# Optimization experiments

Measured on AMD Instinct MI355X. Metric: run time of the kernel, lower is better.

Reference implementation:

```python
import jax, jax.numpy as jnp
import numpy as np

N = 50000
D_IN, D_H1, D_H2 = 256, 128, 64
E = 1_600_000


def setup_inputs() -> dict:
    key = jax.random.key(0)
    k = jax.random.split(key, 6)
    x = jax.random.normal(k[0], (N, D_IN), dtype=jnp.float32)
    edge_index = jax.random.randint(k[1], (2, E), 0, N, dtype=jnp.int64)
    # Glorot-style init like torch_geometric GCNConv (weight [in, out], zero bias)
    W1 = jax.random.normal(k[2], (D_IN, D_H1), dtype=jnp.float32) * (2.0 / (D_IN + D_H1)) ** 0.5
    b1 = jnp.zeros((D_H1,), dtype=jnp.float32)
    W2 = jax.random.normal(k[3], (D_H1, D_H2), dtype=jnp.float32) * (2.0 / (D_H1 + D_H2)) ** 0.5
    b2 = jnp.zeros((D_H2,), dtype=jnp.float32)
    return {"x": x, "edge_index": edge_index, "W1": W1, "b1": b1, "W2": W2, "b2": b2}


def _gcn_norm(edge_index, n):
    # add self-loops, symmetric normalization: D^{-1/2} (A+I) D^{-1/2}
    loops = jnp.arange(n, dtype=edge_index.dtype)
    src = jnp.concatenate([edge_index[0], loops])
    dst = jnp.concatenate([edge_index[1], loops])
    deg = jnp.zeros((n,), jnp.float32).at[dst].add(1.0)
    dinv = jnp.where(deg > 0, jax.lax.rsqrt(deg), 0.0)
    w = dinv[src] * dinv[dst]  # [E+N]
    return src, dst, w


def _gcn_conv(x, W, b, src, dst, w, n):
    z = x @ W  # dense transform first (out_dim < in_dim)
    msg = z[src] * w[:, None]  # gather + scale, [E+N, out]
    out = jax.ops.segment_sum(msg, dst, num_segments=n)  # scatter-add
    return out + b


def reference(x, edge_index, W1, b1, W2, b2):
    src, dst, w = _gcn_norm(edge_index, N)
    z = jax.nn.relu(_gcn_conv(x, W1, b1, src, dst, w, N))
    z = jax.nn.relu(_gcn_conv(z, W2, b2, src, dst, w, N))
    return z
```

## Files before the change

kernel.cpp:

```cpp
#include <hip/hip_runtime.h>
#include <hip/hip_bf16.h>
#include <cstdint>
#include <cstddef>

#define NNODES 50000
#define NEDGES 1600000
#define DIN 256
#define DH1 128
#define DH2 64

#define NBKT 196
#define NCHUNK 128
#define CHUNKE 12500
#define STAGE_CAP 10240

__device__ __forceinline__ float bflo(uint32_t u) { return __uint_as_float(u << 16); }
__device__ __forceinline__ float bfhi(uint32_t u) { return __uint_as_float(u & 0xffff0000u); }
__device__ __forceinline__ uint16_t f2bf(float f) {
    uint32_t u = __float_as_uint(f);
    u += 0x7fffu + ((u >> 16) & 1u);
    return (uint16_t)(u >> 16);
}

using b8 = __attribute__((ext_vector_type(8))) short;
using f4x = __attribute__((ext_vector_type(4))) float;

__global__ __launch_bounds__(256) void k_chunkhist(const int* __restrict__ dst,
                                                   int* __restrict__ counts) {
    __shared__ int hist[NBKT];
    int c = blockIdx.x, t = threadIdx.x;
    if (t < NBKT) hist[t] = 0;
    __syncthreads();
    int e0 = c * CHUNKE, e1 = min(NEDGES, e0 + CHUNKE);
    for (int e = e0 + t; e < e1; e += 256) atomicAdd(&hist[dst[e] >> 8], 1);
    __syncthreads();
    if (t < NBKT) counts[c * NBKT + t] = hist[t];
}

__global__ __launch_bounds__(256) void k_bktscan(int* __restrict__ counts,
                                                 int* __restrict__ bktstart,
                                                 int* __restrict__ bktcnt) {
    __shared__ int lds[256];
    int t = threadIdx.x;
    int total = 0;
    if (t < NBKT)
        for (int c = 0; c < NCHUNK; ++c) total += counts[c * NBKT + t];
    lds[t] = total;
    __syncthreads();
    for (int d = 1; d < 256; d <<= 1) {
        int add = (t >= d) ? lds[t - d] : 0;
        __syncthreads();
        lds[t] += add;
        __syncthreads();
    }
    int base = lds[t] - total;
    if (t < NBKT) {
        bktstart[t] = base;
        bktcnt[t] = total;
        int run = base;
        for (int c = 0; c < NCHUNK; ++c) {
            int x = counts[c * NBKT + t];
            counts[c * NBKT + t] = run;
            run += x;
        }
    }
}

__global__ __launch_bounds__(256) void k_pairscatter(const int* __restrict__ src,
                                                     const int* __restrict__ dst,
                                                     const int* __restrict__ counts,
                                                     uint32_t* __restrict__ pairs) {
    __shared__ int cur[NBKT];
    int c = blockIdx.x, t = threadIdx.x;
    if (t < NBKT) cur[t] = counts[c * NBKT + t];
    __syncthreads();
    int e0 = c * CHUNKE, e1 = min(NEDGES, e0 + CHUNKE);
    for (int e = e0 + t; e < e1; e += 256) {
        int d = dst[e];
        int pos = atomicAdd(&cur[d >> 8], 1);
        pairs[pos] = ((uint32_t)(d & 255) << 16) | (uint32_t)src[e];
    }
}

__global__ __launch_bounds__(256) void k_sortbucket(const uint32_t* __restrict__ pairs,
                                                    const int* __restrict__ bktstart,
                                                    const int* __restrict__ bktcnt,
                                                    int* __restrict__ csr,
                                                    int* __restrict__ off,
                                                    float* __restrict__ dinv) {
    __shared__ int hist[256];
    __shared__ int cur[256];
    __shared__ int stage[STAGE_CAP];
    int b = blockIdx.x, t = threadIdx.x;
    int e0 = bktstart[b], ecnt = bktcnt[b];
    hist[t] = 0;
    __syncthreads();
    for (int e = e0 + t; e < e0 + ecnt; e += 256)
        atomicAdd(&hist[pairs[e] >> 16], 1);
    __syncthreads();
    int v = hist[t];
    cur[t] = v;
    __syncthreads();
    for (int d = 1; d < 256; d <<= 1) {
        int add = (t >= d) ? cur[t - d] : 0;
        __syncthreads();
        cur[t] += add;
        __syncthreads();
    }
    int excl = cur[t] - v;
    int node = (b << 8) + t;
    if (node < NNODES) {
        off[node] = e0 + excl;
        dinv[node] = rsqrtf((float)(v + 1));
    }
    if (b == NBKT - 1 && t == 0) off[NNODES] = NEDGES;
    __syncthreads();
    cur[t] = e0 + excl;
    __syncthreads();
    if (ecnt <= STAGE_CAP) {
        for (int e = e0 + t; e < e0 + ecnt; e += 256) {
            uint32_t p = pairs[e];
            int pos = atomicAdd(&cur[p >> 16], 1);
            stage[pos - e0] = (int)(p & 0xFFFF);
        }
        __syncthreads();
        for (int i = t; i < ecnt; i += 256) csr[e0 + i] = stage[i];
    } else {
        for (int e = e0 + t; e < e0 + ecnt; e += 256) {
            uint32_t p = pairs[e];
            int pos = atomicAdd(&cur[p >> 16], 1);
            csr[pos] = (int)(p & 0xFFFF);
        }
    }
}

template <int K, int NN>
__global__ __launch_bounds__(256) void k_wsplit(const float* __restrict__ W,
                                                uint16_t* __restrict__ Wth,
                                                uint16_t* __restrict__ Wtl) {
    int idx = blockIdx.x * 256 + threadIdx.x;
    if (idx >= K * NN) return;
    int k = idx / NN, n = idx % NN;
    float f = W[idx];
    uint16_t h = f2bf(f);
    uint16_t l = f2bf(f - bflo((uint32_t)h));
    Wth[n * K + k] = h;
    Wtl[n * K + k] = l;
}

template <int K, int NN>
__global__ __launch_bounds__(256) void k_gemm_mfma(const float* __restrict__ X,
                                                   const uint16_t* __restrict__ Wth,
                                                   const uint16_t* __restrict__ Wtl,
                                                   const float* __restrict__ dinv,
                                                   uint16_t* __restrict__ Z) {
    constexpr int BM = 64, BK = 64;
    constexpr int NW = NN / 64;
    __shared__ uint16_t Ah[BM * BK], Al[BM * BK], Wh[NN * BK], Wl[NN * BK];
    const int t = threadIdx.x;
    const int wave = t >> 6, lane = t & 63;
    const int bm = blockIdx.x * BM;
    const int r16 = lane & 15, kg = lane >> 4;
    const int n0 = wave * (NW * 16);
    f4x acc[4][NW] = {};

    for (int k0 = 0; k0 < K; k0 += BK) {
        {
            int row = t >> 2, kq = (t & 3) * 16;
            const float* xp = X + (size_t)(bm + row) * K + k0 + kq;
            bool ok = (bm + row) < NNODES;
            float v[16];
#pragma unroll
            for (int u = 0; u < 4; ++u) {
                float4 f = ok ? *reinterpret_cast<const float4*>(xp + u * 4)
                              : make_float4(0.f, 0.f, 0.f, 0.f);
                v[u * 4 + 0] = f.x; v[u * 4 + 1] = f.y;
                v[u * 4 + 2] = f.z; v[u * 4 + 3] = f.w;
            }
            uint16_t hh[16], ll[16];
#pragma unroll
            for (int u = 0; u < 16; ++u) {
                uint16_t h = f2bf(v[u]);
                hh[u] = h;
                ll[u] = f2bf(v[u] - bflo((uint32_t)h));
            }
#pragma unroll
            for (int j = 0; j < 2; ++j) {
                int s = (t & 3) * 2 + j;
                int idx = (row * 8 + (s ^ (row & 7))) * 8;
                const uint16_t* hp = hh + j * 8;
                const uint16_t* lp = ll + j * 8;
                uint4 ph, pl;
                ph.x = hp[0] | ((uint32_t)hp[1] << 16);
                ph.y = hp[2] | ((uint32_t)hp[3] << 16);
                ph.z = hp[4] | ((uint32_t)hp[5] << 16);
                ph.w = hp[6] | ((uint32_t)hp[7] << 16);
                pl.x = lp[0] | ((uint32_t)lp[1] << 16);
                pl.y = lp[2] | ((uint32_t)lp[3] << 16);
                pl.z = lp[4] | ((uint32_t)lp[5] << 16);
                pl.w = lp[6] | ((uint32_t)lp[7] << 16);
                *reinterpret_cast<uint4*>(&Ah[idx]) = ph;
                *reinterpret_cast<uint4*>(&Al[idx]) = pl;
            }
        }
        {
            constexpr int TPR = 256 / NN;
            constexpr int SPT = 8 / TPR;
            int n = t / TPR, q = t % TPR;
#pragma unroll
            for (int j = 0; j < SPT; ++j) {
                int s = q * SPT + j;
                uint4 vh = *reinterpret_cast<const uint4*>(&Wth[(size_t)n * K + k0 + s * 8]);
                uint4 vl = *reinterpret_cast<const uint4*>(&Wtl[(size_t)n * K + k0 + s * 8]);
                int idx = (n * 8 + (s ^ (n & 7))) * 8;
                *reinterpret_cast<uint4*>(&Wh[idx]) = vh;
                *reinterpret_cast<uint4*>(&Wl[idx]) = vl;
            }
        }
        __syncthreads();
#pragma unroll
        for (int ks = 0; ks < 2; ++ks) {
            int kslot = ks * 4 + kg;
            b8 a_h[4], a_l[4];
#pragma unroll
            for (int mt = 0; mt < 4; ++mt) {
                int row = mt * 16 + r16;
                int idx = (row * 8 + (kslot ^ (row & 7))) * 8;
                a_h[mt] = *reinterpret_cast<const b8*>(&Ah[idx]);
                a_l[mt] = *reinterpret_cast<const b8*>(&Al[idx]);
            }
            b8 b_h[NW], b_l[NW];
#pragma unroll
            for (int nt = 0; nt < NW; ++nt) {
                int n = n0 + nt * 16 + r16;
                int idx = (n * 8 + (kslot ^ (n & 7))) * 8;
                b_h[nt] = *reinterpret_cast<const b8*>(&Wh[idx]);
                b_l[nt] = *reinterpret_cast<const b8*>(&Wl[idx]);
            }
#pragma unroll
            for (int mt = 0; mt < 4; ++mt)
#pragma unroll
                for (int nt = 0; nt < NW; ++nt) {
                    acc[mt][nt] = __builtin_amdgcn_mfma_f32_16x16x32_bf16(
                        a_h[mt], b_h[nt], acc[mt][nt], 0, 0, 0);
                    acc[mt][nt] = __builtin_amdgcn_mfma_f32_16x16x32_bf16(
                        a_h[mt], b_l[nt], acc[mt][nt], 0, 0, 0);
                    acc[mt][nt] = __builtin_amdgcn_mfma_f32_16x16x32_bf16(
                        a_l[mt], b_h[nt], acc[mt][nt], 0, 0, 0);
                }
        }
        __syncthreads();
    }
#pragma unroll
    for (int mt = 0; mt < 4; ++mt) {
#pragma unroll
        for (int i = 0; i < 4; ++i) {
            int m = bm + mt * 16 + kg * 4 + i;
            if (m < NNODES) {
                float di = dinv[m];
#pragma unroll
                for (int nt = 0; nt < NW; ++nt) {
                    int n = n0 + nt * 16 + r16;
                    Z[(size_t)m * NN + n] = f2bf(acc[mt][nt][i] * di);
                }
            }
        }
    }
}

template <int D>
__global__ __launch_bounds__(256) void k_agg_bf(const uint16_t* __restrict__ zs,
                                                const int* __restrict__ csr,
                                                const int* __restrict__ off,
                                                const float* __restrict__ dinv,
                                                const float* __restrict__ bias,
                                                float* __restrict__ out) {
    int wid = (blockIdx.x * 256 + threadIdx.x) >> 6;
    int lane = threadIdx.x & 63;
    if (wid >= NNODES) return;
    int start = off[wid];
    int c = off[wid + 1] - start;
    float di = dinv[wid];
    if constexpr (D == 128) {
        const uint32_t* Z = reinterpret_cast<const uint32_t*>(zs);
        uint32_t us = Z[(size_t)wid * 64 + lane];
        float ax = bflo(us), ay = bfhi(us);
        float bx = 0, by = 0, cx = 0, cy = 0, dx = 0, dy = 0;
        int j = 0;
        for (; j + 3 < c; j += 4) {
            int s0 = csr[start + j], s1 = csr[start + j + 1];
            int s2 = csr[start + j + 2], s3 = csr[start + j + 3];
            uint32_t u0 = Z[(size_t)s0 * 64 + lane];
            uint32_t u1 = Z[(size_t)s1 * 64 + lane];
            uint32_t u2 = Z[(size_t)s2 * 64 + lane];
            uint32_t u3 = Z[(size_t)s3 * 64 + lane];
            ax += bflo(u0); ay += bfhi(u0);
            bx += bflo(u1); by += bfhi(u1);
            cx += bflo(u2); cy += bfhi(u2);
            dx += bflo(u3); dy += bfhi(u3);
        }
        for (; j < c; ++j) {
            uint32_t u = Z[(size_t)csr[start + j] * 64 + lane];
            ax += bflo(u); ay += bfhi(u);
        }
        float sx = (ax + bx) + (cx + dx);
        float sy = (ay + by) + (cy + dy);
        float2 bv = *reinterpret_cast<const float2*>(bias + lane * 2);
        float2 o;
        o.x = fmaxf(fmaf(sx, di, bv.x), 0.f);
        o.y = fmaxf(fmaf(sy, di, bv.y), 0.f);
        *reinterpret_cast<float2*>(out + (size_t)wid * 128 + lane * 2) = o;
    } else {
        float a = __uint_as_float(((uint32_t)zs[(size_t)wid * 64 + lane]) << 16);
        float b = 0, cc = 0, d = 0;
        int j = 0;
        for (; j + 3 < c; j += 4) {
            int s0 = csr[start + j], s1 = csr[start + j + 1];
            int s2 = csr[start + j + 2], s3 = csr[start + j + 3];
            a += __uint_as_float(((uint32_t)zs[(size_t)s0 * 64 + lane]) << 16);
            b += __uint_as_float(((uint32_t)zs[(size_t)s1 * 64 + lane]) << 16);
            cc += __uint_as_float(((uint32_t)zs[(size_t)s2 * 64 + lane]) << 16);
            d += __uint_as_float(((uint32_t)zs[(size_t)s3 * 64 + lane]) << 16);
        }
        for (; j < c; ++j)
            a += __uint_as_float(((uint32_t)zs[(size_t)csr[start + j] * 64 + lane]) << 16);
        float s = (a + b) + (cc + d);
        float o = fmaxf(fmaf(s, di, bias[lane]), 0.f);
        out[(size_t)wid * 64 + lane] = o;
    }
}

extern "C" void kernel_launch(void* const* d_in, const int* in_sizes, int n_in,
                              void* d_out, int out_size, void* d_ws, size_t ws_size,
                              hipStream_t stream) {
    const float* x = (const float*)d_in[0];
    const int* ei = (const int*)d_in[1];
    const float* W1 = (const float*)d_in[2];
    const float* b1 = (const float*)d_in[3];
    const float* W2 = (const float*)d_in[4];
    const float* b2 = (const float*)d_in[5];
    float* out = (float*)d_out;

    char* ws = (char*)d_ws;
    int* counts = (int*)(ws + 0);
    int* bktstart = (int*)(ws + 101376);
    int* bktcnt = (int*)(ws + 102400);
    int* off = (int*)(ws + 103424);
    float* dinv = (float*)(ws + 303616);
    int* csr = (int*)(ws + 503808);
    uint16_t* zs1 = (uint16_t*)(ws + 6904832);
    uint16_t* wt1h = (uint16_t*)(ws + 19705856);
    uint16_t* wt1l = (uint16_t*)(ws + 19771392);
    uint16_t* wt2h = (uint16_t*)(ws + 19836928);
    uint16_t* wt2l = (uint16_t*)(ws + 19853312);
    float* h1 = (float*)(ws + 19870720);
    uint32_t* pairs = (uint32_t*)h1;
    uint16_t* zs2 = zs1;

    const int* esrc = ei;
    const int* edst = ei + NEDGES;

    k_wsplit<DIN, DH1><<<(DIN * DH1 + 255) / 256, 256, 0, stream>>>(W1, wt1h, wt1l);
    k_wsplit<DH1, DH2><<<(DH1 * DH2 + 255) / 256, 256, 0, stream>>>(W2, wt2h, wt2l);

    k_chunkhist<<<NCHUNK, 256, 0, stream>>>(edst, counts);
    k_bktscan<<<1, 256, 0, stream>>>(counts, bktstart, bktcnt);
    k_pairscatter<<<NCHUNK, 256, 0, stream>>>(esrc, edst, counts, pairs);
    k_sortbucket<<<NBKT, 256, 0, stream>>>(pairs, bktstart, bktcnt, csr, off, dinv);

    int gm = (NNODES + 63) / 64;
    k_gemm_mfma<DIN, DH1><<<gm, 256, 0, stream>>>(x, wt1h, wt1l, dinv, zs1);
    k_agg_bf<DH1><<<NNODES / 4, 256, 0, stream>>>(zs1, csr, off, dinv, b1, h1);

    k_gemm_mfma<DH1, DH2><<<gm, 256, 0, stream>>>(h1, wt2h, wt2l, dinv, zs2);
    k_agg_bf<DH2><<<NNODES / 4, 256, 0, stream>>>(zs2, csr, off, dinv, b2, out);
}
```

Before: 316.8 us.

## Fuse CSR build preprocessing into three kernels with redundant per-block scans

Merges the two weight-split kernels into the chunk histogram kernel, and removes the single-block bucket scan kernel. Each pair-scatter and sort-bucket block now recomputes the bucket totals and prefix sums from the counts array itself. The chunk count rises to 196 so the fused first kernel covers all weight elements. This cuts the launch count from six to three and drops a serial single-block step, at the cost of every block redundantly reading the 196x196 counts matrix.

Result: faster. 310.5 us (-2.0%).

```diff
diff --git a/kernel.cpp b/kernel.cpp
--- a/kernel.cpp
+++ b/kernel.cpp
@@ -10,8 +10,8 @@
 #define DH2 64
 
 #define NBKT 196
-#define NCHUNK 128
-#define CHUNKE 12500
+#define NCHUNK 196
+#define CHUNKE 8164
 #define STAGE_CAP 10240
 
 __device__ __forceinline__ float bflo(uint32_t u) { return __uint_as_float(u << 16); }
@@ -25,56 +25,68 @@
 using b8 = __attribute__((ext_vector_type(8))) short;
 using f4x = __attribute__((ext_vector_type(4))) float;
 
-__global__ __launch_bounds__(256) void k_chunkhist(const int* __restrict__ dst,
-                                                   int* __restrict__ counts) {
-    __shared__ int hist[NBKT];
-    int c = blockIdx.x, t = threadIdx.x;
-    if (t < NBKT) hist[t] = 0;
-    __syncthreads();
-    int e0 = c * CHUNKE, e1 = min(NEDGES, e0 + CHUNKE);
+__global__ __launch_bounds__(256) void k_pre1(const float* __restrict__ W1g,
+                                              const float* __restrict__ W2g,
+                                              uint16_t* __restrict__ wt1h,
+                                              uint16_t* __restrict__ wt1l,
+                                              uint16_t* __restrict__ wt2h,
+                                              uint16_t* __restrict__ wt2l,
+                                              const int* __restrict__ dst,
+                                              int* __restrict__ counts) {
+    __shared__ int hist[256];
+    const int b = blockIdx.x, t = threadIdx.x;
+    {
+        int gid = b * 256 + t;
+        if (gid < DIN * DH1) {
+            int k = gid / DH1, n = gid % DH1;
+            float f = W1g[gid];
+            uint16_t h = f2bf(f);
+            wt1h[n * DIN + k] = h;
+            wt1l[n * DIN + k] = f2bf(f - bflo((uint32_t)h));
+        } else if (gid < DIN * DH1 + DH1 * DH2) {
+            int i2 = gid - DIN * DH1;
+            int k = i2 / DH2, n = i2 % DH2;
+            float f = W2g[i2];
+            uint16_t h = f2bf(f);
+            wt2h[n * DH1 + k] = h;
+            wt2l[n * DH1 + k] = f2bf(f - bflo((uint32_t)h));
+        }
+    }
+    hist[t] = 0;
+    __syncthreads();
+    const int e0 = b * CHUNKE, e1 = min(NEDGES, e0 + CHUNKE);
     for (int e = e0 + t; e < e1; e += 256) atomicAdd(&hist[dst[e] >> 8], 1);
     __syncthreads();
-    if (t < NBKT) counts[c * NBKT + t] = hist[t];
-}
-
-__global__ __launch_bounds__(256) void k_bktscan(int* __restrict__ counts,
-                                                 int* __restrict__ bktstart,
-                                                 int* __restrict__ bktcnt) {
-    __shared__ int lds[256];
-    int t = threadIdx.x;
-    int total = 0;
-    if (t < NBKT)
-        for (int c = 0; c < NCHUNK; ++c) total += counts[c * NBKT + t];
-    lds[t] = total;
+    if (t < NBKT) counts[b * NBKT + t] = hist[t];
+}
+
+__global__ __launch_bounds__(256) void k_pre2(const int* __restrict__ src,
+                                              const int* __restrict__ dst,
+                                              const int* __restrict__ counts,
+                                              uint32_t* __restrict__ pairs) {
+    __shared__ int cur[256];
+    const int b = blockIdx.x, t = threadIdx.x;
+    int tot = 0, myprefix = 0;
+    if (t < NBKT) {
+        for (int c = 0; c < NCHUNK; ++c) {
+            int v = counts[c * NBKT + t];
+            tot += v;
+            if (c < b) myprefix += v;
+        }
+    }
+    cur[t] = tot;
     __syncthreads();
     for (int d = 1; d < 256; d <<= 1) {
-        int add = (t >= d) ? lds[t - d] : 0;
-        __syncthreads();
-        lds[t] += add;
-        __syncthreads();
-    }
-    int base = lds[t] - total;
-    if (t < NBKT) {
-        bktstart[t] = base;
-        bktcnt[t] = total;
-        int run = base;
-        for (int c = 0; c < NCHUNK; ++c) {
-            int x = counts[c * NBKT + t];
-            counts[c * NBKT + t] = run;
-            run += x;
-        }
-    }
-}
-
-__global__ __launch_bounds__(256) void k_pairscatter(const int* __restrict__ src,
-                                                     const int* __restrict__ dst,
-                                                     const int* __restrict__ counts,
-                                                     uint32_t* __restrict__ pairs) {
-    __shared__ int cur[NBKT];
-    int c = blockIdx.x, t = threadIdx.x;
-    if (t < NBKT) cur[t] = counts[c * NBKT + t];
-    __syncthreads();
-    int e0 = c * CHUNKE, e1 = min(NEDGES, e0 + CHUNKE);
+        int add = (t >= d) ? cur[t - d] : 0;
+        __syncthreads();
+        cur[t] += add;
+        __syncthreads();
+    }
+    int base = cur[t] - tot + myprefix;
+    __syncthreads();
+    cur[t] = base;
+    __syncthreads();
+    const int e0 = b * CHUNKE, e1 = min(NEDGES, e0 + CHUNKE);
     for (int e = e0 + t; e < e1; e += 256) {
         int d = dst[e];
         int pos = atomicAdd(&cur[d >> 8], 1);
@@ -82,20 +94,34 @@
     }
 }
 
-__global__ __launch_bounds__(256) void k_sortbucket(const uint32_t* __restrict__ pairs,
-                                                    const int* __restrict__ bktstart,
-                                                    const int* __restrict__ bktcnt,
-                                                    int* __restrict__ csr,
-                                                    int* __restrict__ off,
-                                                    float* __restrict__ dinv) {
+__global__ __launch_bounds__(256) void k_pre3(const uint32_t* __restrict__ pairs,
+                                              const int* __restrict__ counts,
+                                              int* __restrict__ csr,
+                                              int* __restrict__ off,
+                                              float* __restrict__ dinv) {
     __shared__ int hist[256];
     __shared__ int cur[256];
     __shared__ int stage[STAGE_CAP];
-    int b = blockIdx.x, t = threadIdx.x;
-    int e0 = bktstart[b], ecnt = bktcnt[b];
+    const int b = blockIdx.x, t = threadIdx.x;
+    int tot = 0;
+    if (t < NBKT)
+        for (int c = 0; c < NCHUNK; ++c) tot += counts[c * NBKT + t];
+    cur[t] = tot;
+    __syncthreads();
+    for (int d = 1; d < 256; d <<= 1) {
+        int add = (t >= d) ? cur[t - d] : 0;
+        __syncthreads();
+        cur[t] += add;
+        __syncthreads();
+    }
+    hist[t] = cur[t] - tot;
+    stage[t] = tot;
+    __syncthreads();
+    const int be0 = hist[b], ecnt = stage[b];
+    __syncthreads();
     hist[t] = 0;
     __syncthreads();
-    for (int e = e0 + t; e < e0 + ecnt; e += 256)
+    for (int e = be0 + t; e < be0 + ecnt; e += 256)
         atomicAdd(&hist[pairs[e] >> 16], 1);
     __syncthreads();
     int v = hist[t];
@@ -110,42 +136,28 @@
     int excl = cur[t] - v;
     int node = (b << 8) + t;
     if (node < NNODES) {
-        off[node] = e0 + excl;
+        off[node] = be0 + excl;
         dinv[node] = rsqrtf((float)(v + 1));
     }
-    if (b == NBKT - 1 && t == 0) off[NNODES] = NEDGES;
-    __syncthreads();
-    cur[t] = e0 + excl;
+    if (b == 0 && t == 0) off[NNODES] = NEDGES;
+    __syncthreads();
+    cur[t] = be0 + excl;
     __syncthreads();
     if (ecnt <= STAGE_CAP) {
-        for (int e = e0 + t; e < e0 + ecnt; e += 256) {
+        for (int e = be0 + t; e < be0 + ecnt; e += 256) {
             uint32_t p = pairs[e];
             int pos = atomicAdd(&cur[p >> 16], 1);
-            stage[pos - e0] = (int)(p & 0xFFFF);
-        }
-        __syncthreads();
-        for (int i = t; i < ecnt; i += 256) csr[e0 + i] = stage[i];
+            stage[pos - be0] = (int)(p & 0xFFFF);
+        }
+        __syncthreads();
+        for (int i = t; i < ecnt; i += 256) csr[be0 + i] = stage[i];
     } else {
-        for (int e = e0 + t; e < e0 + ecnt; e += 256) {
+        for (int e = be0 + t; e < be0 + ecnt; e += 256) {
             uint32_t p = pairs[e];
             int pos = atomicAdd(&cur[p >> 16], 1);
             csr[pos] = (int)(p & 0xFFFF);
         }
     }
-}
-
-template <int K, int NN>
-__global__ __launch_bounds__(256) void k_wsplit(const float* __restrict__ W,
-                                                uint16_t* __restrict__ Wth,
-                                                uint16_t* __restrict__ Wtl) {
-    int idx = blockIdx.x * 256 + threadIdx.x;
-    if (idx >= K * NN) return;
-    int k = idx / NN, n = idx % NN;
-    float f = W[idx];
-    uint16_t h = f2bf(f);
-    uint16_t l = f2bf(f - bflo((uint32_t)h));
-    Wth[n * K + k] = h;
-    Wtl[n * K + k] = l;
 }
 
 template <int K, int NN>
@@ -343,30 +355,24 @@
 
     char* ws = (char*)d_ws;
     int* counts = (int*)(ws + 0);
-    int* bktstart = (int*)(ws + 101376);
-    int* bktcnt = (int*)(ws + 102400);
-    int* off = (int*)(ws + 103424);
-    float* dinv = (float*)(ws + 303616);
-    int* csr = (int*)(ws + 503808);
-    uint16_t* zs1 = (uint16_t*)(ws + 6904832);
-    uint16_t* wt1h = (uint16_t*)(ws + 19705856);
-    uint16_t* wt1l = (uint16_t*)(ws + 19771392);
-    uint16_t* wt2h = (uint16_t*)(ws + 19836928);
-    uint16_t* wt2l = (uint16_t*)(ws + 19853312);
-    float* h1 = (float*)(ws + 19870720);
+    int* off = (int*)(ws + 156672);
+    float* dinv = (float*)(ws + 357376);
+    int* csr = (int*)(ws + 557568);
+    uint16_t* zs1 = (uint16_t*)(ws + 6957568);
+    uint16_t* wt1h = (uint16_t*)(ws + 19757568);
+    uint16_t* wt1l = (uint16_t*)(ws + 19823104);
+    uint16_t* wt2h = (uint16_t*)(ws + 19888640);
+    uint16_t* wt2l = (uint16_t*)(ws + 19905024);
+    float* h1 = (float*)(ws + 19921408);
     uint32_t* pairs = (uint32_t*)h1;
     uint16_t* zs2 = zs1;
 
     const int* esrc = ei;
     const int* edst = ei + NEDGES;
 
-    k_wsplit<DIN, DH1><<<(DIN * DH1 + 255) / 256, 256, 0, stream>>>(W1, wt1h, wt1l);
-    k_wsplit<DH1, DH2><<<(DH1 * DH2 + 255) / 256, 256, 0, stream>>>(W2, wt2h, wt2l);
-
-    k_chunkhist<<<NCHUNK, 256, 0, stream>>>(edst, counts);
-    k_bktscan<<<1, 256, 0, stream>>>(counts, bktstart, bktcnt);
-    k_pairscatter<<<NCHUNK, 256, 0, stream>>>(esrc, edst, counts, pairs);
-    k_sortbucket<<<NBKT, 256, 0, stream>>>(pairs, bktstart, bktcnt, csr, off, dinv);
+    k_pre1<<<NCHUNK, 256, 0, stream>>>(W1, W2, wt1h, wt1l, wt2h, wt2l, edst, counts);
+    k_pre2<<<NCHUNK, 256, 0, stream>>>(esrc, edst, counts, pairs);
+    k_pre3<<<NBKT, 256, 0, stream>>>(pairs, counts, csr, off, dinv);
 
     int gm = (NNODES + 63) / 64;
     k_gemm_mfma<DIN, DH1><<<gm, 256, 0, stream>>>(x, wt1h, wt1l, dinv, zs1);
```
